# Kernel optimization log

Hardware: AMD Instinct MI355X
Metric: run time of the kernel (lower is better)

## Reference

```python
import jax, jax.numpy as jnp
import numpy as np

VOCAB_PRI = 100000
VOCAB_SEC = 100000
EMBED_DIM = 64


def setup_inputs() -> dict:
    key = jax.random.key(0)
    k1, k2, k3, k4 = jax.random.split(key, 4)
    inputs_pri = jax.random.randint(k1, (4096, 200), 0, VOCAB_PRI, dtype=jnp.int64 if jax.config.jax_enable_x64 else jnp.int32)
    inputs_sec = jax.random.randint(k2, (4096, 200), 0, VOCAB_SEC, dtype=jnp.int64 if jax.config.jax_enable_x64 else jnp.int32)
    initrange = 0.01
    emb_pri = jax.random.uniform(k3, (VOCAB_PRI, EMBED_DIM), jnp.float32, -initrange, initrange)
    emb_sec = jax.random.uniform(k4, (VOCAB_SEC, EMBED_DIM), jnp.float32, -initrange, initrange)
    return {"inputs_pri": inputs_pri, "inputs_sec": inputs_sec,
            "emb_pri": emb_pri, "emb_sec": emb_sec}


def _embed_sum(table, idx):
    # gather [B, S, D] then sum over sentence dim -> [B, D]
    # (equivalent to cAdd's per-token accumulation / EmbeddingBag(sum))
    return jnp.sum(table[idx], axis=1)


def reference(inputs_pri, inputs_sec, emb_pri, emb_sec):
    out_pri = _embed_sum(emb_pri, inputs_pri)  # [B, D]
    out_sec = _embed_sum(emb_sec, inputs_sec)  # [B, D]
    return out_pri, out_sec
```

## Files before the change

### kernel.cpp

```cpp
#include <hip/hip_runtime.h>
#include <hip/hip_bf16.h>


#define BB 4096
#define SS 200
#define DD 64
#define VOCAB 100000

typedef float vfloat4 __attribute__((ext_vector_type(4)));

__global__ __launch_bounds__(256) void convert_bf16(
    const float* __restrict__ src,
    uint2* __restrict__ dst)
{
    const size_t g = (size_t)blockIdx.x * 256 + threadIdx.x;
    const float4 v = ((const float4*)src)[g];
    const unsigned u0 = __bfloat16_as_ushort(__float2bfloat16(v.x));
    const unsigned u1 = __bfloat16_as_ushort(__float2bfloat16(v.y));
    const unsigned u2 = __bfloat16_as_ushort(__float2bfloat16(v.z));
    const unsigned u3 = __bfloat16_as_ushort(__float2bfloat16(v.w));
    uint2 o;
    o.x = u0 | (u1 << 16);
    o.y = u2 | (u3 << 16);
    dst[g] = o;
}

__global__ __launch_bounds__(256) void embed_sum_bf16(
    const int* __restrict__ idx,
    const uint2* __restrict__ emb,
    float* __restrict__ out)
{
    __shared__ int sidx[2][SS];
    __shared__ float4 wred[2][16];

    const int tid  = (int)threadIdx.x;
    const int w    = tid >> 6;
    const int lane = tid & 63;
    const int p    = w >> 1;
    const int h    = w & 1;
    const int b    = (int)blockIdx.x * 2 + p;

    const int* ib = idx + (size_t)blockIdx.x * 2 * SS;
    if (tid < (2 * SS) / 4) {
        const int4 v = ((const int4*)ib)[tid];
        int* s = &sidx[0][0];
        s[tid * 4 + 0] = v.x;
        s[tid * 4 + 1] = v.y;
        s[tid * 4 + 2] = v.z;
        s[tid * 4 + 3] = v.w;
    }
    __syncthreads();

    const int q   = lane >> 4;
    const int l16 = lane & 15;

    float4 acc = make_float4(0.f, 0.f, 0.f, 0.f);

    #pragma unroll 5
    for (int k = 0; k < 25; ++k) {
        const int i = sidx[p][8 * k + 4 * h + q];
        const uint2 v = emb[(size_t)i * 16 + l16];
        acc.x += __uint_as_float(v.x << 16);
        acc.y += __uint_as_float(v.x & 0xffff0000u);
        acc.z += __uint_as_float(v.y << 16);
        acc.w += __uint_as_float(v.y & 0xffff0000u);
    }

    acc.x += __shfl_down(acc.x, 32);
    acc.y += __shfl_down(acc.y, 32);
    acc.z += __shfl_down(acc.z, 32);
    acc.w += __shfl_down(acc.w, 32);
    acc.x += __shfl_down(acc.x, 16);
    acc.y += __shfl_down(acc.y, 16);
    acc.z += __shfl_down(acc.z, 16);
    acc.w += __shfl_down(acc.w, 16);

    if (h == 1 && lane < 16) wred[p][l16] = acc;
    __syncthreads();
    if (h == 0 && lane < 16) {
        const float4 o = wred[p][l16];
        acc.x += o.x; acc.y += o.y; acc.z += o.z; acc.w += o.w;
        ((float4*)(out + (size_t)b * DD))[l16] = acc;
    }
}

__global__ __launch_bounds__(256) void bilingual_embed_sum(
    const int* __restrict__ idx_pri,
    const int* __restrict__ idx_sec,
    const float* __restrict__ emb_pri,
    const float* __restrict__ emb_sec,
    float* __restrict__ out)
{
    __shared__ int sidx[4][SS];
    const int w    = (int)(threadIdx.x >> 6);
    const int lane = (int)(threadIdx.x & 63);
    const int wave = (int)(blockIdx.x * 4 + w);
    const int table = wave >> 12;
    const int b     = wave & (BB - 1);

    const int*   idx = table ? idx_sec : idx_pri;
    const float* emb = table ? emb_sec : emb_pri;
    float* outp = out + (size_t)table * BB * DD + (size_t)b * DD;

    const int* row_idx = idx + b * SS;
    if (lane < SS / 4) {
        const int4 v = ((const int4*)row_idx)[lane];
        sidx[w][lane * 4 + 0] = v.x;
        sidx[w][lane * 4 + 1] = v.y;
        sidx[w][lane * 4 + 2] = v.z;
        sidx[w][lane * 4 + 3] = v.w;
    }
    __syncthreads();

    const int q   = lane >> 4;
    const int l16 = lane & 15;
    float4 acc = make_float4(0.f, 0.f, 0.f, 0.f);

    #pragma unroll 10
    for (int s0 = 0; s0 < SS; s0 += 4) {
        const int i = sidx[w][s0 + q];
        const float4 v = ((const float4*)(emb + (size_t)i * DD))[l16];
        acc.x += v.x; acc.y += v.y; acc.z += v.z; acc.w += v.w;
    }

    acc.x += __shfl_down(acc.x, 32);
    acc.y += __shfl_down(acc.y, 32);
    acc.z += __shfl_down(acc.z, 32);
    acc.w += __shfl_down(acc.w, 32);
    acc.x += __shfl_down(acc.x, 16);
    acc.y += __shfl_down(acc.y, 16);
    acc.z += __shfl_down(acc.z, 16);
    acc.w += __shfl_down(acc.w, 16);

    if (lane < 16) ((float4*)outp)[l16] = acc;
}

extern "C" void kernel_launch(void* const* d_in, const int* in_sizes, int n_in,
                              void* d_out, int out_size, void* d_ws, size_t ws_size,
                              hipStream_t stream) {
    const int*   idx_pri = (const int*)d_in[0];
    const int*   idx_sec = (const int*)d_in[1];
    const float* emb_pri = (const float*)d_in[2];
    const float* emb_sec = (const float*)d_in[3];
    float* out = (float*)d_out;

    const size_t ws_need = (size_t)VOCAB * DD * 2;

    if (ws_size >= ws_need) {
        uint2* tbl = (uint2*)d_ws;
        const int conv_grid   = (VOCAB * DD / 4) / 256;
        const int gather_grid = BB / 2;

        convert_bf16<<<conv_grid, 256, 0, stream>>>(emb_pri, tbl);
        embed_sum_bf16<<<gather_grid, 256, 0, stream>>>(idx_pri, tbl, out);
        convert_bf16<<<conv_grid, 256, 0, stream>>>(emb_sec, tbl);
        embed_sum_bf16<<<gather_grid, 256, 0, stream>>>(idx_sec, tbl,
                                                        out + (size_t)BB * DD);
    } else {
        bilingual_embed_sum<<<(2 * BB) / 4, 256, 0, stream>>>(
            idx_pri, idx_sec, emb_pri, emb_sec, out);
    }
}
```

Baseline: 123.4 us.

## Merge both tables' bf16 conversion and gather into single launches

Converts both embedding tables to bf16 in one kernel, writing to separate workspace regions, with nontemporal loads and stores. It then gathers and sums both tables in one kernel that assigns one wave per output row, dropping the two-wave split and its shared-memory reduction. This cuts four launches to two and gives each launch more parallel work, at the cost of twice the workspace. If the workspace is too small, the code falls back to the fp32 path.

Result: no change. 123.6 us (+0.2%).

```diff
diff --git a/kernel.cpp b/kernel.cpp
--- a/kernel.cpp
+++ b/kernel.cpp
@@ -6,60 +6,67 @@
 #define SS 200
 #define DD 64
 #define VOCAB 100000
+#define TBL_U2 ((size_t)VOCAB * DD / 4)
 
-typedef float vfloat4 __attribute__((ext_vector_type(4)));
+typedef float    vfloat4 __attribute__((ext_vector_type(4)));
+typedef unsigned vuint2  __attribute__((ext_vector_type(2)));
 
-__global__ __launch_bounds__(256) void convert_bf16(
-    const float* __restrict__ src,
-    uint2* __restrict__ dst)
+__global__ __launch_bounds__(256) void convert_both(
+    const float* __restrict__ src_pri,
+    const float* __restrict__ src_sec,
+    vuint2* __restrict__ dst)
 {
-    const size_t g = (size_t)blockIdx.x * 256 + threadIdx.x;
-    const float4 v = ((const float4*)src)[g];
+    const int per_table = (VOCAB * DD / 4) / 256;
+    const int t = (int)blockIdx.x >= per_table;
+    const size_t g = ((size_t)blockIdx.x - (size_t)t * per_table) * 256 + threadIdx.x;
+
+    const float* src = t ? src_sec : src_pri;
+    const vfloat4 v = __builtin_nontemporal_load((const vfloat4*)src + g);
     const unsigned u0 = __bfloat16_as_ushort(__float2bfloat16(v.x));
     const unsigned u1 = __bfloat16_as_ushort(__float2bfloat16(v.y));
     const unsigned u2 = __bfloat16_as_ushort(__float2bfloat16(v.z));
     const unsigned u3 = __bfloat16_as_ushort(__float2bfloat16(v.w));
-    uint2 o;
+    vuint2 o;
     o.x = u0 | (u1 << 16);
     o.y = u2 | (u3 << 16);
-    dst[g] = o;
+    __builtin_nontemporal_store(o, dst + (size_t)t * TBL_U2 + g);
 }
 
-__global__ __launch_bounds__(256) void embed_sum_bf16(
-    const int* __restrict__ idx,
-    const uint2* __restrict__ emb,
+__global__ __launch_bounds__(256) void gather_both(
+    const int* __restrict__ idx_pri,
+    const int* __restrict__ idx_sec,
+    const vuint2* __restrict__ emb,
     float* __restrict__ out)
 {
-    __shared__ int sidx[2][SS];
-    __shared__ float4 wred[2][16];
+    __shared__ int sidx[4][SS];
 
     const int tid  = (int)threadIdx.x;
     const int w    = tid >> 6;
     const int lane = tid & 63;
-    const int p    = w >> 1;
-    const int h    = w & 1;
-    const int b    = (int)blockIdx.x * 2 + p;
+    const int wave = (int)blockIdx.x * 4 + w;
+    const int t    = wave >> 12;
+    const int b    = wave & (BB - 1);
 
-    const int* ib = idx + (size_t)blockIdx.x * 2 * SS;
-    if (tid < (2 * SS) / 4) {
-        const int4 v = ((const int4*)ib)[tid];
-        int* s = &sidx[0][0];
-        s[tid * 4 + 0] = v.x;
-        s[tid * 4 + 1] = v.y;
-        s[tid * 4 + 2] = v.z;
-        s[tid * 4 + 3] = v.w;
+    const int* row_idx = (t ? idx_sec : idx_pri) + b * SS;
+    if (lane < SS / 4) {
+        const int4 v = ((const int4*)row_idx)[lane];
+        sidx[w][lane * 4 + 0] = v.x;
+        sidx[w][lane * 4 + 1] = v.y;
+        sidx[w][lane * 4 + 2] = v.z;
+        sidx[w][lane * 4 + 3] = v.w;
     }
     __syncthreads();
 
     const int q   = lane >> 4;
     const int l16 = lane & 15;
+    const vuint2* et = emb + (size_t)t * TBL_U2;
 
     float4 acc = make_float4(0.f, 0.f, 0.f, 0.f);
 
-    #pragma unroll 5
-    for (int k = 0; k < 25; ++k) {
-        const int i = sidx[p][8 * k + 4 * h + q];
-        const uint2 v = emb[(size_t)i * 16 + l16];
+    #pragma unroll 10
+    for (int s0 = 0; s0 < SS; s0 += 4) {
+        const int i = sidx[w][s0 + q];
+        const vuint2 v = et[(size_t)i * 16 + l16];
         acc.x += __uint_as_float(v.x << 16);
         acc.y += __uint_as_float(v.x & 0xffff0000u);
         acc.z += __uint_as_float(v.y << 16);
@@ -75,12 +82,8 @@
     acc.z += __shfl_down(acc.z, 16);
     acc.w += __shfl_down(acc.w, 16);
 
-    if (h == 1 && lane < 16) wred[p][l16] = acc;
-    __syncthreads();
-    if (h == 0 && lane < 16) {
-        const float4 o = wred[p][l16];
-        acc.x += o.x; acc.y += o.y; acc.z += o.z; acc.w += o.w;
-        ((float4*)(out + (size_t)b * DD))[l16] = acc;
+    if (lane < 16) {
+        ((float4*)(out + ((size_t)t * BB + b) * DD))[l16] = acc;
     }
 }
 
@@ -144,18 +147,15 @@
     const float* emb_sec = (const float*)d_in[3];
     float* out = (float*)d_out;
 
-    const size_t ws_need = (size_t)VOCAB * DD * 2;
+    const size_t ws_need = (size_t)2 * VOCAB * DD * 2;
 
     if (ws_size >= ws_need) {
-        uint2* tbl = (uint2*)d_ws;
-        const int conv_grid   = (VOCAB * DD / 4) / 256;
-        const int gather_grid = BB / 2;
+        vuint2* tbl = (vuint2*)d_ws;
+        const int conv_grid   = 2 * (VOCAB * DD / 4) / 256;
+        const int gather_grid = (2 * BB) / 4;
 
-        convert_bf16<<<conv_grid, 256, 0, stream>>>(emb_pri, tbl);
-        embed_sum_bf16<<<gather_grid, 256, 0, stream>>>(idx_pri, tbl, out);
-        convert_bf16<<<conv_grid, 256, 0, stream>>>(emb_sec, tbl);
-        embed_sum_bf16<<<gather_grid, 256, 0, stream>>>(idx_sec, tbl,
-                                                        out + (size_t)BB * DD);
+        convert_both<<<conv_grid, 256, 0, stream>>>(emb_pri, emb_sec, tbl);
+        gather_both<<<gather_grid, 256, 0, stream>>>(idx_pri, idx_sec, tbl, out);
     } else {
         bilingual_embed_sum<<<(2 * BB) / 4, 256, 0, stream>>>(
             idx_pri, idx_sec, emb_pri, emb_sec, out);
```
